# Performance work log

Measured on AMD Instinct MI355X. Metric: run time of the kernel, lower is better.

## Reference

```python
import jax, jax.numpy as jnp
import numpy as np

GRID_SIZE = 128  # D = H = W
N_POINTS = 8388608


def setup_inputs() -> dict:
    key = jax.random.key(0)
    k_grid, k_coords = jax.random.split(key)
    # occupancy grid buffer: binary {0,1} values as float, shape [D, H, W]
    grid = (jax.random.uniform(k_grid, (GRID_SIZE, GRID_SIZE, GRID_SIZE)) > 0.5).astype(jnp.float32)
    # normalized [-1, 1] query coordinates, layout [..., 3] = (x, y, z)
    coords = jax.random.uniform(k_coords, (N_POINTS, 3), minval=-1.0, maxval=1.0, dtype=jnp.float32)
    return {"grid": grid, "coords": coords}


def _trilinear_sample(grid, coords):
    """torch.nn.functional.grid_sample 5D, mode='bilinear', align_corners=False,
    padding_mode='zeros'. grid: [D,H,W]; coords: [N,3] with (x,y,z) where
    x indexes W, y indexes H, z indexes D. Returns [N]."""
    D, H, W = grid.shape
    x, y, z = coords[:, 0], coords[:, 1], coords[:, 2]
    # unnormalize (align_corners=False): pixel = ((c + 1) * size - 1) / 2
    ix = ((x + 1.0) * W - 1.0) * 0.5
    iy = ((y + 1.0) * H - 1.0) * 0.5
    iz = ((z + 1.0) * D - 1.0) * 0.5

    ix0 = jnp.floor(ix)
    iy0 = jnp.floor(iy)
    iz0 = jnp.floor(iz)
    wx = ix - ix0  # fractional weights
    wy = iy - iy0
    wz = iz - iz0
    ix0 = ix0.astype(jnp.int32)
    iy0 = iy0.astype(jnp.int32)
    iz0 = iz0.astype(jnp.int32)

    def gather(zi, yi, xi):
        # zero padding: out-of-bounds corners contribute 0
        valid = ((zi >= 0) & (zi < D) & (yi >= 0) & (yi < H) & (xi >= 0) & (xi < W))
        zc = jnp.clip(zi, 0, D - 1)
        yc = jnp.clip(yi, 0, H - 1)
        xc = jnp.clip(xi, 0, W - 1)
        return jnp.where(valid, grid[zc, yc, xc], 0.0)

    out = (
        gather(iz0,     iy0,     ix0    ) * (1 - wz) * (1 - wy) * (1 - wx)
        + gather(iz0,     iy0,     ix0 + 1) * (1 - wz) * (1 - wy) * wx
        + gather(iz0,     iy0 + 1, ix0    ) * (1 - wz) * wy       * (1 - wx)
        + gather(iz0,     iy0 + 1, ix0 + 1) * (1 - wz) * wy       * wx
        + gather(iz0 + 1, iy0,     ix0    ) * wz       * (1 - wy) * (1 - wx)
        + gather(iz0 + 1, iy0,     ix0 + 1) * wz       * (1 - wy) * wx
        + gather(iz0 + 1, iy0 + 1, ix0    ) * wz       * wy       * (1 - wx)
        + gather(iz0 + 1, iy0 + 1, ix0 + 1) * wz       * wy       * wx
    )
    return out


def reference(grid, coords):
    flat = coords.reshape(-1, 3)
    return _trilinear_sample(grid, flat)
```

## Files before the change

kernel.cpp:

```cpp
#include <hip/hip_runtime.h>


typedef float fx4 __attribute__((ext_vector_type(4)));
typedef unsigned int u32;
typedef unsigned long long u64;

constexpr int GS = 128;
constexpr int TD = GS + 1;
constexpr size_t MASK_BYTES = (size_t)GS * GS * GS / 8;
constexpr size_t TBL_BYTES  = (size_t)TD * TD * TD;
constexpr size_t WS_NEW = MASK_BYTES;
constexpr size_t WS_FB  = MASK_BYTES + TBL_BYTES + 64;

constexpr int NP_MAX = 65;
constexpr size_t SLAB_LDS = (size_t)NP_MAX * 2048 + 16;

__global__ __launch_bounds__(256)
void bitpack_kernel(const float* __restrict__ grid, u64* __restrict__ mask) {
    int gid = blockIdx.x * blockDim.x + threadIdx.x;
    float v = grid[gid];
    u64 m = __ballot(v != 0.0f);
    if ((threadIdx.x & 63) == 0) mask[gid >> 6] = m;
}

__global__ __launch_bounds__(1024, 4)
void sample_slab(const u32* __restrict__ mask32,
                 const float* __restrict__ coords,
                 float* __restrict__ out, int npts) {
    extern __shared__ u32 lds[];
    const int tid = threadIdx.x;
    const int nthr = 1024;
    const int ptsPerBlock = npts / gridDim.x;
    const int base = blockIdx.x * ptsPerBlock;
    const int ngroups = ptsPerBlock / (4 * nthr);
    const fx4* c4 = (const fx4*)coords;

#pragma unroll 1
    for (int s = 0; s < 2; ++s) {
        const int pz0 = s ? 63 : 0;
        const int np  = s ? 65 : 64;
        const int zlo = s ? 64 : 0;
        const int zhi = s ? 128 : 63;
        __syncthreads();
        {
            const int nwords = np * 512;
            const u32* src = mask32 + pz0 * 512;
            for (int i = tid; i < nwords; i += nthr) lds[i] = src[i];
            if (tid == 0) lds[nwords] = 0;
        }
        __syncthreads();

        for (int g = 0; g < ngroups; ++g) {
            int grp = base / 4 + g * nthr + tid;
            fx4 q0 = c4[3 * grp + 0];
            fx4 q1 = c4[3 * grp + 1];
            fx4 q2 = c4[3 * grp + 2];
            float f[12] = {q0.x, q0.y, q0.z, q0.w,
                           q1.x, q1.y, q1.z, q1.w,
                           q2.x, q2.y, q2.z, q2.w};
#pragma unroll
            for (int j = 0; j < 4; ++j) {
                float ixf = fmaf(f[3 * j + 0], 64.0f, 63.5f);
                float iyf = fmaf(f[3 * j + 1], 64.0f, 63.5f);
                float izf = fmaf(f[3 * j + 2], 64.0f, 63.5f);
                float fxx = floorf(ixf), fyy = floorf(iyf), fzz = floorf(izf);
                float wx = ixf - fxx, wy = iyf - fyy, wz = izf - fzz;
                int x0 = (int)fxx, y0 = (int)fyy, z0 = (int)fzz;
                int zb = z0 + 1;
                if (zb >= zlo && zb <= zhi) {
                    int xc = x0 < 0 ? 0 : x0;
                    int k  = xc >> 5;
                    int p0 = x0 - (k << 5);
                    u32 okx0 = (u32)(x0 >= 0);
                    u32 okx1 = (u32)(x0 <= 126);
                    float r[2][2];
#pragma unroll
                    for (int dz = 0; dz < 2; ++dz) {
                        int zl = z0 + dz - pz0;
                        u32 vz = (u32)((unsigned)zl < (unsigned)np);
#pragma unroll
                        for (int dy = 0; dy < 2; ++dy) {
                            int yr = y0 + dy;
                            u32 v = vz & (u32)((unsigned)yr < 128u);
                            int widx = v ? (zl * 128 + yr) * 4 + k : 0;
                            u32 w0 = lds[widx];
                            u32 w1 = lds[widx + 1];
                            u64 vv = (u64)w0 | ((u64)w1 << 32);
                            int b0 = (int)((u32)(vv >> (p0 & 63)) & 1u & okx0 & v);
                            int b1 = (int)((u32)(vv >> ((p0 + 1) & 63)) & 1u & okx1 & v);
                            r[dz][dy] = fmaf(wx, (float)(b1 - b0), (float)b0);
                        }
                    }
                    float c0 = fmaf(wy, r[0][1] - r[0][0], r[0][0]);
                    float c1 = fmaf(wy, r[1][1] - r[1][0], r[1][0]);
                    out[grp * 4 + j] = fmaf(wz, c1 - c0, c0);
                }
            }
        }
    }
}

__device__ __forceinline__ unsigned bit_at(u64 lo, u64 hi, int xi) {
    if ((unsigned)xi >= 128u) return 0u;
    u64 w = (xi < 64) ? lo : hi;
    return (unsigned)((w >> (xi & 63)) & 1ull);
}

__global__ __launch_bounds__(256)
void table_kernel(const u64* __restrict__ mask, unsigned char* __restrict__ tbl) {
    int i = blockIdx.x * blockDim.x + threadIdx.x;
    if (i >= (int)TBL_BYTES) return;
    int x = i % TD;
    int t = i / TD;
    int y = t % TD;
    int z = t / TD;
    int x0 = x - 1;
    unsigned byte = 0u;
#pragma unroll
    for (int dz = 0; dz < 2; ++dz) {
#pragma unroll
        for (int dy = 0; dy < 2; ++dy) {
            int yi = y - 1 + dy, zi = z - 1 + dz;
            u64 lo = 0ull, hi = 0ull;
            if (((unsigned)yi < 128u) & ((unsigned)zi < 128u)) {
                int r = (zi * 128 + yi) * 2;
                lo = mask[r];
                hi = mask[r + 1];
            }
            int kk = dy * 2 + dz * 4;
            byte |= (bit_at(lo, hi, x0) << kk) | (bit_at(lo, hi, x0 + 1) << (kk + 1));
        }
    }
    tbl[i] = (unsigned char)byte;
}

__global__ __launch_bounds__(256)
void sample_packed(const unsigned char* __restrict__ tbl,
                   const float* __restrict__ coords,
                   float* __restrict__ out, int nt) {
    int t = blockIdx.x * blockDim.x + threadIdx.x;
    if (t >= nt) return;
    const fx4* c4 = (const fx4*)coords;
    fx4 q[6];
#pragma unroll
    for (int j = 0; j < 6; ++j) q[j] = c4[6 * t + j];
    const float* f = (const float*)q;
    float wxa[8], wya[8], wza[8];
    int addr[8];
#pragma unroll
    for (int i = 0; i < 8; ++i) {
        float ix = fmaf(f[3 * i + 0], 64.0f, 63.5f);
        float iy = fmaf(f[3 * i + 1], 64.0f, 63.5f);
        float iz = fmaf(f[3 * i + 2], 64.0f, 63.5f);
        float fx = floorf(ix), fy = floorf(iy), fz = floorf(iz);
        wxa[i] = ix - fx; wya[i] = iy - fy; wza[i] = iz - fz;
        int xb = (int)fx + 1, yb = (int)fy + 1, zb = (int)fz + 1;
        addr[i] = (zb * TD + yb) * TD + xb;
    }
    unsigned bytes[8];
#pragma unroll
    for (int i = 0; i < 8; ++i) bytes[i] = (unsigned)tbl[addr[i]];
    float o[8];
#pragma unroll
    for (int i = 0; i < 8; ++i) {
        unsigned byte = bytes[i];
        float wx = wxa[i], wy = wya[i], wz = wza[i];
        float v0 = (float)( byte       & 1u);
        float v1 = (float)((byte >> 1) & 1u);
        float v2 = (float)((byte >> 2) & 1u);
        float v3 = (float)((byte >> 3) & 1u);
        float v4 = (float)((byte >> 4) & 1u);
        float v5 = (float)((byte >> 5) & 1u);
        float v6 = (float)((byte >> 6) & 1u);
        float v7 = (float)((byte >> 7) & 1u);
        float c00 = v0 + wx * (v1 - v0);
        float c10 = v2 + wx * (v3 - v2);
        float c01 = v4 + wx * (v5 - v4);
        float c11 = v6 + wx * (v7 - v6);
        float c0  = c00 + wy * (c10 - c00);
        float c1  = c01 + wy * (c11 - c01);
        o[i] = c0 + wz * (c1 - c0);
    }
    fx4* o4 = (fx4*)out;
    fx4 r0 = {o[0], o[1], o[2], o[3]};
    fx4 r1 = {o[4], o[5], o[6], o[7]};
    o4[2 * t + 0] = r0;
    o4[2 * t + 1] = r1;
}

extern "C" void kernel_launch(void* const* d_in, const int* in_sizes, int n_in,
                              void* d_out, int out_size, void* d_ws, size_t ws_size,
                              hipStream_t stream) {
    const float* grid   = (const float*)d_in[0];
    const float* coords = (const float*)d_in[1];
    float* out = (float*)d_out;
    int npts = in_sizes[1] / 3;

    u64* mask = (u64*)d_ws;
    int vox = GS * GS * GS;

    (void)hipFuncSetAttribute((const void*)sample_slab,
                              hipFuncAttributeMaxDynamicSharedMemorySize,
                              (int)SLAB_LDS);
    int nb = 0;
    hipError_t oe = hipOccupancyMaxActiveBlocksPerMultiprocessor(
        &nb, sample_slab, 1024, SLAB_LDS);
    bool slab_ok = (oe == hipSuccess) && (nb >= 1) && (ws_size >= WS_NEW) &&
                   (npts % (256 * 4096) == 0);

    if (slab_ok) {
        bitpack_kernel<<<vox / 256, 256, 0, stream>>>(grid, mask);
        sample_slab<<<256, 1024, SLAB_LDS, stream>>>((const u32*)mask, coords, out, npts);
    } else if (ws_size >= WS_FB) {
        unsigned char* tbl = (unsigned char*)d_ws + MASK_BYTES;
        bitpack_kernel<<<vox / 256, 256, 0, stream>>>(grid, mask);
        int tbl_blocks = (int)((TBL_BYTES + 255) / 256);
        table_kernel<<<tbl_blocks, 256, 0, stream>>>(mask, tbl);
        int nt = npts / 8;
        sample_packed<<<(nt + 255) / 256, 256, 0, stream>>>(tbl, coords, out, nt);
    }
}
```

Before: 201.5 us.

## Use zero-padded bitmask and three LDS slabs with coords loaded once

Adds a kernel that builds a zero-padded, x-shifted bitmask so sampling can skip bounds checks and read corner bits with one funnel shift. The sampler now reads each thread's 8 points into registers once. It then sweeps three z-slabs of 46 planes through LDS, which is smaller than the previous two-slab layout and allows more resident blocks. This removes the repeated coordinate reads and out-of-bounds masking of the old two-pass version, at the cost of an extra preprocessing launch and a third slab load per block. The fast path now applies only when the point count is exactly 8M.

```diff
diff --git a/kernel.cpp b/kernel.cpp
--- a/kernel.cpp
+++ b/kernel.cpp
@@ -3,17 +3,26 @@
 
 typedef float fx4 __attribute__((ext_vector_type(4)));
 typedef unsigned int u32;
+typedef unsigned int ux4 __attribute__((ext_vector_type(4)));
 typedef unsigned long long u64;
 
 constexpr int GS = 128;
+constexpr int PROW_W  = 5;
+constexpr int PPLANE_W = 130 * PROW_W;
+constexpr int PMASK_WORDS = 130 * PPLANE_W;
+constexpr size_t PMASK_BYTES = (size_t)PMASK_WORDS * 4;
+
+constexpr size_t MASK_BYTES = (size_t)GS * GS * GS / 8;
+constexpr size_t MASK_OFF   = (PMASK_BYTES + 63) & ~(size_t)63;
+constexpr size_t WS_MAIN    = MASK_OFF + MASK_BYTES;
+
 constexpr int TD = GS + 1;
-constexpr size_t MASK_BYTES = (size_t)GS * GS * GS / 8;
-constexpr size_t TBL_BYTES  = (size_t)TD * TD * TD;
-constexpr size_t WS_NEW = MASK_BYTES;
-constexpr size_t WS_FB  = MASK_BYTES + TBL_BYTES + 64;
-
-constexpr int NP_MAX = 65;
-constexpr size_t SLAB_LDS = (size_t)NP_MAX * 2048 + 16;
+constexpr size_t TBL_BYTES = (size_t)TD * TD * TD;
+constexpr size_t TBL_OFF   = MASK_OFF + MASK_BYTES;
+constexpr size_t WS_FB     = TBL_OFF + TBL_BYTES;
+
+constexpr int SLAB_ALLOC_WORDS = 46 * PPLANE_W + 1;
+constexpr size_t SLAB_LDS = (size_t)SLAB_ALLOC_WORDS * 4;
 
 __global__ __launch_bounds__(256)
 void bitpack_kernel(const float* __restrict__ grid, u64* __restrict__ mask) {
@@ -23,81 +32,100 @@
     if ((threadIdx.x & 63) == 0) mask[gid >> 6] = m;
 }
 
+__global__ __launch_bounds__(256)
+void padmask_kernel(const u32* __restrict__ mask32, u32* __restrict__ pmask) {
+    int i = blockIdx.x * blockDim.x + threadIdx.x;
+    if (i >= PMASK_WORDS) return;
+    int k = i % PROW_W;
+    int r = i / PROW_W;
+    int py = r % 130;
+    int pz = r / 130;
+    int y = py - 1, z = pz - 1;
+    u32 w = 0;
+    if (((unsigned)y < 128u) & ((unsigned)z < 128u)) {
+        const u32* vrow = mask32 + (z * 128 + y) * 4;
+        u32 lo = (k >= 1) ? vrow[k - 1] : 0u;
+        u32 hi = (k < 4) ? vrow[k] : 0u;
+        w = (lo >> 31) | (hi << 1);
+    }
+    pmask[i] = w;
+}
+
 __global__ __launch_bounds__(1024, 4)
-void sample_slab(const u32* __restrict__ mask32,
-                 const float* __restrict__ coords,
-                 float* __restrict__ out, int npts) {
+void sample_slab3(const u32* __restrict__ pmask,
+                  const float* __restrict__ coords,
+                  float* __restrict__ out) {
     extern __shared__ u32 lds[];
     const int tid = threadIdx.x;
-    const int nthr = 1024;
-    const int ptsPerBlock = npts / gridDim.x;
-    const int base = blockIdx.x * ptsPerBlock;
-    const int ngroups = ptsPerBlock / (4 * nthr);
+    const int T = blockIdx.x * 1024 + tid;
     const fx4* c4 = (const fx4*)coords;
+    fx4 q[6];
+#pragma unroll
+    for (int j = 0; j < 6; ++j) q[j] = c4[6 * T + j];
+    const float* f = (const float*)q;
+
+    u32 pr[8];
+    float wx[8], wy[8], wz[8], o[8];
+#pragma unroll
+    for (int j = 0; j < 8; ++j) {
+        float ix = fmaf(f[3 * j + 0], 64.0f, 63.5f);
+        float iy = fmaf(f[3 * j + 1], 64.0f, 63.5f);
+        float iz = fmaf(f[3 * j + 2], 64.0f, 63.5f);
+        float fx = floorf(ix), fy = floorf(iy), fz = floorf(iz);
+        wx[j] = ix - fx; wy[j] = iy - fy; wz[j] = iz - fz;
+        int X  = (int)fx + 1;
+        int Y  = (int)fy + 1;
+        int PZ = (int)fz + 1;
+        int k = X >> 5, p = X & 31;
+        u32 R = (u32)((PZ * 130 + Y) * PROW_W + k);
+        pr[j] = R | ((u32)p << 20) | ((u32)PZ << 25);
+        o[j] = 0.0f;
+    }
 
 #pragma unroll 1
-    for (int s = 0; s < 2; ++s) {
-        const int pz0 = s ? 63 : 0;
-        const int np  = s ? 65 : 64;
-        const int zlo = s ? 64 : 0;
-        const int zhi = s ? 128 : 63;
+    for (int s = 0; s < 3; ++s) {
+        const int p0 = (s == 0) ? 0 : (s == 1 ? 44 : 88);
+        const int np = (s == 2) ? 42 : 46;
+        const int lo = (s == 0) ? 0 : (s == 1 ? 45 : 89);
+        const int hi = (s == 0) ? 44 : (s == 1 ? 88 : 128);
         __syncthreads();
         {
-            const int nwords = np * 512;
-            const u32* src = mask32 + pz0 * 512;
-            for (int i = tid; i < nwords; i += nthr) lds[i] = src[i];
-            if (tid == 0) lds[nwords] = 0;
+            const int nv = np * PPLANE_W / 4;
+            const ux4* src = (const ux4*)(pmask + p0 * PPLANE_W);
+            ux4* dst = (ux4*)lds;
+            for (int i = tid; i < nv; i += 1024) dst[i] = src[i];
         }
         __syncthreads();
-
-        for (int g = 0; g < ngroups; ++g) {
-            int grp = base / 4 + g * nthr + tid;
-            fx4 q0 = c4[3 * grp + 0];
-            fx4 q1 = c4[3 * grp + 1];
-            fx4 q2 = c4[3 * grp + 2];
-            float f[12] = {q0.x, q0.y, q0.z, q0.w,
-                           q1.x, q1.y, q1.z, q1.w,
-                           q2.x, q2.y, q2.z, q2.w};
-#pragma unroll
-            for (int j = 0; j < 4; ++j) {
-                float ixf = fmaf(f[3 * j + 0], 64.0f, 63.5f);
-                float iyf = fmaf(f[3 * j + 1], 64.0f, 63.5f);
-                float izf = fmaf(f[3 * j + 2], 64.0f, 63.5f);
-                float fxx = floorf(ixf), fyy = floorf(iyf), fzz = floorf(izf);
-                float wx = ixf - fxx, wy = iyf - fyy, wz = izf - fzz;
-                int x0 = (int)fxx, y0 = (int)fyy, z0 = (int)fzz;
-                int zb = z0 + 1;
-                if (zb >= zlo && zb <= zhi) {
-                    int xc = x0 < 0 ? 0 : x0;
-                    int k  = xc >> 5;
-                    int p0 = x0 - (k << 5);
-                    u32 okx0 = (u32)(x0 >= 0);
-                    u32 okx1 = (u32)(x0 <= 126);
-                    float r[2][2];
-#pragma unroll
-                    for (int dz = 0; dz < 2; ++dz) {
-                        int zl = z0 + dz - pz0;
-                        u32 vz = (u32)((unsigned)zl < (unsigned)np);
-#pragma unroll
-                        for (int dy = 0; dy < 2; ++dy) {
-                            int yr = y0 + dy;
-                            u32 v = vz & (u32)((unsigned)yr < 128u);
-                            int widx = v ? (zl * 128 + yr) * 4 + k : 0;
-                            u32 w0 = lds[widx];
-                            u32 w1 = lds[widx + 1];
-                            u64 vv = (u64)w0 | ((u64)w1 << 32);
-                            int b0 = (int)((u32)(vv >> (p0 & 63)) & 1u & okx0 & v);
-                            int b1 = (int)((u32)(vv >> ((p0 + 1) & 63)) & 1u & okx1 & v);
-                            r[dz][dy] = fmaf(wx, (float)(b1 - b0), (float)b0);
-                        }
-                    }
-                    float c0 = fmaf(wy, r[0][1] - r[0][0], r[0][0]);
-                    float c1 = fmaf(wy, r[1][1] - r[1][0], r[1][0]);
-                    out[grp * 4 + j] = fmaf(wz, c1 - c0, c0);
-                }
-            }
+#pragma unroll
+        for (int j = 0; j < 8; ++j) {
+            int PZ = (int)(pr[j] >> 25);
+            if ((unsigned)(PZ - lo) > (unsigned)(hi - lo)) continue;
+            int p  = (int)((pr[j] >> 20) & 31u);
+            int rb = (int)(pr[j] & 0xFFFFFu) - p0 * PPLANE_W;
+            int rb2 = rb + PPLANE_W;
+            u32 a0 = lds[rb],      a1 = lds[rb + 1];
+            u32 b0 = lds[rb + 5],  b1 = lds[rb + 6];
+            u32 c0 = lds[rb2],     c1 = lds[rb2 + 1];
+            u32 d0 = lds[rb2 + 5], d1 = lds[rb2 + 6];
+            u32 t00 = (u32)((((u64)a1 << 32) | a0) >> p) & 3u;
+            u32 t01 = (u32)((((u64)b1 << 32) | b0) >> p) & 3u;
+            u32 t10 = (u32)((((u64)c1 << 32) | c0) >> p) & 3u;
+            u32 t11 = (u32)((((u64)d1 << 32) | d0) >> p) & 3u;
+            float w = wx[j];
+            float r00 = fmaf(w, (float)(t00 >> 1) - (float)(t00 & 1u), (float)(t00 & 1u));
+            float r01 = fmaf(w, (float)(t01 >> 1) - (float)(t01 & 1u), (float)(t01 & 1u));
+            float r10 = fmaf(w, (float)(t10 >> 1) - (float)(t10 & 1u), (float)(t10 & 1u));
+            float r11 = fmaf(w, (float)(t11 >> 1) - (float)(t11 & 1u), (float)(t11 & 1u));
+            float cy0 = fmaf(wy[j], r01 - r00, r00);
+            float cy1 = fmaf(wy[j], r11 - r10, r10);
+            o[j] = fmaf(wz[j], cy1 - cy0, cy0);
         }
     }
+    fx4* o4 = (fx4*)out;
+    fx4 r0 = {o[0], o[1], o[2], o[3]};
+    fx4 r1 = {o[4], o[5], o[6], o[7]};
+    o4[2 * T]     = r0;
+    o4[2 * T + 1] = r1;
 }
 
 __device__ __forceinline__ unsigned bit_at(u64 lo, u64 hi, int xi) {
@@ -195,27 +223,28 @@
     const float* coords = (const float*)d_in[1];
     float* out = (float*)d_out;
     int npts = in_sizes[1] / 3;
-
-    u64* mask = (u64*)d_ws;
     int vox = GS * GS * GS;
 
-    (void)hipFuncSetAttribute((const void*)sample_slab,
+    u32* pmask = (u32*)d_ws;
+    u64* mask  = (u64*)((char*)d_ws + MASK_OFF);
+
+    (void)hipFuncSetAttribute((const void*)sample_slab3,
                               hipFuncAttributeMaxDynamicSharedMemorySize,
                               (int)SLAB_LDS);
     int nb = 0;
     hipError_t oe = hipOccupancyMaxActiveBlocksPerMultiprocessor(
-        &nb, sample_slab, 1024, SLAB_LDS);
-    bool slab_ok = (oe == hipSuccess) && (nb >= 1) && (ws_size >= WS_NEW) &&
-                   (npts % (256 * 4096) == 0);
+        &nb, sample_slab3, 1024, SLAB_LDS);
+    bool slab_ok = (oe == hipSuccess) && (nb >= 1) && (ws_size >= WS_MAIN) &&
+                   (npts == 1024 * 1024 * 8);
 
     if (slab_ok) {
         bitpack_kernel<<<vox / 256, 256, 0, stream>>>(grid, mask);
-        sample_slab<<<256, 1024, SLAB_LDS, stream>>>((const u32*)mask, coords, out, npts);
+        padmask_kernel<<<(PMASK_WORDS + 255) / 256, 256, 0, stream>>>((const u32*)mask, pmask);
+        sample_slab3<<<1024, 1024, SLAB_LDS, stream>>>(pmask, coords, out);
     } else if (ws_size >= WS_FB) {
-        unsigned char* tbl = (unsigned char*)d_ws + MASK_BYTES;
+        unsigned char* tbl = (unsigned char*)d_ws + TBL_OFF;
         bitpack_kernel<<<vox / 256, 256, 0, stream>>>(grid, mask);
-        int tbl_blocks = (int)((TBL_BYTES + 255) / 256);
-        table_kernel<<<tbl_blocks, 256, 0, stream>>>(mask, tbl);
+        table_kernel<<<(int)((TBL_BYTES + 255) / 256), 256, 0, stream>>>(mask, tbl);
         int nt = npts / 8;
         sample_packed<<<(nt + 255) / 256, 256, 0, stream>>>(tbl, coords, out, nt);
     }
```

New measurement: 194.7 us. 1.03x faster.
